# Performance work log

Measured on AMD Instinct MI355X. Metric: run time of the kernel, lower is better.

The kernel has to match this reference:

```python
import jax, jax.numpy as jnp
import numpy as np

H, D, K, FF = 8, 512, 64, 64  # n_head, feature_dim, key_feature_dim, dim_feedforward
L, B = 512, 32
LN_EPS = 1e-5


def _l2norm(x, eps=1e-12):
    # torch F.normalize: x / max(||x||, eps)
    n = jnp.sqrt(jnp.sum(x * x, axis=-1, keepdims=True))
    return x / jnp.maximum(n, eps)


def _layernorm(x, g, b, eps=LN_EPS):
    m = jnp.mean(x, axis=-1, keepdims=True)
    v = jnp.mean((x - m) ** 2, axis=-1, keepdims=True)
    return (x - m) * jax.lax.rsqrt(v + eps) * g + b


def setup_inputs() -> dict:
    key0 = jax.random.key(0)
    ks = jax.random.split(key0, 13)
    n = jax.random.normal
    s_kq = float(np.sqrt(2.0 / K))
    s_v = float(np.sqrt(2.0 / D))
    return {
        "query": n(ks[0], (L, B, D), jnp.float32),
        "key": n(ks[1], (L, B, D), jnp.float32),
        "value": n(ks[2], (L, B, D), jnp.float32),
        "WK": n(ks[3], (H, K, D), jnp.float32) * s_kq,
        "WQ": n(ks[4], (H, K, D), jnp.float32) * s_kq,
        "WV": n(ks[5], (H, D, D), jnp.float32) * s_v,
        "Wt": n(ks[6], (H, D, D), jnp.float32) * 0.04,  # trans_conv (default kaiming-ish scale)
        "W1": n(ks[7], (H, FF, D), jnp.float32) * 0.04,
        "b1": jnp.zeros((H, FF), jnp.float32),
        "W2": n(ks[8], (H, D, FF), jnp.float32) * 0.1,
        "b2": jnp.zeros((H, D), jnp.float32),
        "ln_g": jnp.ones((H, D), jnp.float32),
        "ln_b": jnp.zeros((H, D), jnp.float32),
    }


def reference(query, key, value, WK, WQ, WV, Wt, W1, b1, W2, b2, ln_g, ln_b):
    # query/key/value: [L, B, D]; per-head weights stacked on leading H axis.
    Lq, Bb, Dd = query.shape
    Hh = WK.shape[0]

    # per-head cosine-normalized Q/K projections: [H, B, L, K]
    wq = _l2norm(jnp.einsum('lbd,hkd->hblk', query, WQ))
    wk = _l2norm(jnp.einsum('lbd,hkd->hblk', key, WK))

    # attention scores [H, B, Lq, Lk], temp = 1
    dot = jnp.einsum('hbqc,hbkc->hbqk', wq, wk)
    aff = jax.nn.softmax(dot, axis=-1)
    # custom renorm: divide by column sums over the QUERY axis
    aff = aff / (1e-9 + jnp.sum(aff, axis=2, keepdims=True))

    wv = jnp.einsum('lbd,hed->hble', value, WV)        # [H, B, Lk, D]
    out = jnp.einsum('hbqk,hbke->hbqe', aff, wv)       # [H, B, Lq, D]
    out = jnp.transpose(out, (0, 2, 1, 3))             # [H, L, B, D]

    # residual-style trans_conv(query - out) -> relu
    o = jax.nn.relu(jnp.einsum('hlbd,hed->hlbe', query[None] - out, Wt))

    # TransNonlinear FFN (dropout = identity at eval)
    hff = jax.nn.relu(jnp.einsum('hlbd,hfd->hlbf', o, W1) + b1[:, None, None, :])
    s2 = jnp.einsum('hlbf,hdf->hlbd', hff, W2) + b2[:, None, None, :]
    x = _layernorm(o + s2, ln_g[:, None, None, :], ln_b[:, None, None, :])

    # concat heads on last dim, head 0 first: [L, B, H*D]
    return jnp.transpose(x, (1, 2, 0, 3)).reshape(Lq, Bb, Hh * Dd)
```

## Files before the change

### kernel.cpp

```cpp
#include <hip/hip_runtime.h>
#include <stdint.h>

#define HH 8
#define DDIM 512
#define KHEAD 64
#define FFD 64
#define LLEN 512
#define BBATCH 32
#define NTOK 16384

typedef unsigned short u16;
typedef __attribute__((ext_vector_type(8))) __bf16 bf16x8;
typedef __attribute__((ext_vector_type(4))) float f32x4;

__device__ __forceinline__ float bf2f(u16 u) {
    union { uint32_t i; float f; } v; v.i = ((uint32_t)u) << 16; return v.f;
}
__device__ __forceinline__ u16 f2bf(float f) {
    union { uint32_t i; float f; } v; v.f = f;
    return (u16)((v.i + 0x7FFFu + ((v.i >> 16) & 1u)) >> 16);
}

__device__ __forceinline__ void gload16(const void* g, void* l) {
    __builtin_amdgcn_global_load_lds(
        (const __attribute__((address_space(1))) void*)g,
        (__attribute__((address_space(3))) void*)l, 16, 0, 0);
}

struct ConvJob { const float* s; u16* d; int n4; };
struct ConvJobs { ConvJob j[6]; int nj; };

__global__ __launch_bounds__(256) void conv_multi(ConvJobs jobs) {
    for (int k = 0; k < jobs.nj; ++k) {
        const float* s = jobs.j[k].s;
        u16* d = jobs.j[k].d;
        const int n4 = jobs.j[k].n4;
        for (long i = (long)blockIdx.x * 256 + threadIdx.x; i < n4;
             i += (long)gridDim.x * 256) {
            float4 v = ((const float4*)s)[i];
            ushort4 o;
            o.x = f2bf(v.x); o.y = f2bf(v.y); o.z = f2bf(v.z); o.w = f2bf(v.w);
            ((ushort4*)d)[i] = o;
        }
    }
}

enum { M_PLAIN = 0, M_WQK = 1, M_SUBAUX = 2, M_RELU = 3, M_ADDAUX = 4, M_SCALECOL = 5 };

template<int MODE, int ZMAP, int SWAPXY>
__global__ __launch_bounds__(512) void mgemm256(
    const u16* __restrict__ A, const u16* __restrict__ B, u16* __restrict__ C,
    int Kd, int lda, int ldb, int ldc,
    long Ash, long Asb, long Bsh, long Bsb, long Csh, long Csb, int nB2,
    const float* __restrict__ bias, int biasN,
    const void* __restrict__ auxp, long auxsh, long auxsb, int auxld)
{
    __shared__ u16 As[2][256 * 64];
    __shared__ u16 Bs[2][256 * 64];

    const int z = blockIdx.z;
    int h2, b2;
    if (ZMAP == 0)      { h2 = z / nB2;      b2 = z % nB2; }
    else if (ZMAP == 1) { h2 = z & 7;        b2 = z >> 3; }
    else                { h2 = (z >> 3) & 7; b2 = ((z >> 6) << 3) | (z & 7); }
    const int bx = SWAPXY ? blockIdx.y : blockIdx.x;
    const int by = SWAPXY ? blockIdx.x : blockIdx.y;
    const int m0 = bx * 256, n0 = by * 256;
    const u16* Ab = A + h2 * Ash + b2 * Asb + (long)m0 * lda;
    const u16* Bb = B + h2 * Bsh + b2 * Bsb + (long)n0 * ldb;

    const int t = threadIdx.x;
    const int lane = t & 63;
    const int w = t >> 6;
    const int wm = w >> 2;
    const int wn = w & 3;
    const int l15 = lane & 15;
    const int g = lane >> 4;

    f32x4 acc[8][4];
    #pragma unroll
    for (int mf = 0; mf < 8; ++mf)
        #pragma unroll
        for (int nf = 0; nf < 4; ++nf)
            #pragma unroll
            for (int i = 0; i < 4; ++i) acc[mf][nf][i] = 0.f;

    auto stageT = [&](int buf, int k0) {
        #pragma unroll
        for (int c = 0; c < 4; ++c) {
            const int idx = c * 8192 + t * 16;
            const int row = idx >> 7;
            const int g0 = (idx >> 4) & 7;
            gload16((const char*)(Ab + (long)row * lda + k0) + ((g0 ^ (row & 7)) << 4),
                    (char*)As[buf] + c * 8192 + w * 1024);
        }
        #pragma unroll
        for (int c = 0; c < 4; ++c) {
            const int idx = c * 8192 + t * 16;
            const int row = idx >> 7;
            const int g0 = (idx >> 4) & 7;
            gload16((const char*)(Bb + (long)row * ldb + k0) + ((g0 ^ (row & 7)) << 4),
                    (char*)Bs[buf] + c * 8192 + w * 1024);
        }
    };

    stageT(0, 0);
    const int nt = Kd >> 6;
    for (int T = 0; T < nt; ++T) {
        asm volatile("s_waitcnt vmcnt(0)" ::: "memory");
        __builtin_amdgcn_sched_barrier(0);
        __builtin_amdgcn_s_barrier();
        __builtin_amdgcn_sched_barrier(0);
        if (T + 1 < nt) stageT((T + 1) & 1, (T + 1) << 6);

        const char* Abase = (const char*)As[T & 1];
        const char* Bbase = (const char*)Bs[T & 1];
        #pragma unroll
        for (int q = 0; q < 4; ++q) {
            const int mh = q >> 1, nh = q & 1;
            bf16x8 af[4][2], bfv[2][2];
            #pragma unroll
            for (int mf = 0; mf < 4; ++mf) {
                const int row = wm * 128 + (mh * 4 + mf) * 16 + l15;
                #pragma unroll
                for (int kk = 0; kk < 2; ++kk)
                    af[mf][kk] = *(const bf16x8*)(Abase + row * 128 +
                                      (((kk * 4 + g) ^ (row & 7)) << 4));
            }
            #pragma unroll
            for (int nf = 0; nf < 2; ++nf) {
                const int row = wn * 64 + (nh * 2 + nf) * 16 + l15;
                #pragma unroll
                for (int kk = 0; kk < 2; ++kk)
                    bfv[nf][kk] = *(const bf16x8*)(Bbase + row * 128 +
                                      (((kk * 4 + g) ^ (row & 7)) << 4));
            }
            __builtin_amdgcn_s_setprio(1);
            #pragma unroll
            for (int kk = 0; kk < 2; ++kk)
                #pragma unroll
                for (int mf = 0; mf < 4; ++mf)
                    #pragma unroll
                    for (int nf = 0; nf < 2; ++nf)
                        acc[mh * 4 + mf][nh * 2 + nf] =
                            __builtin_amdgcn_mfma_f32_16x16x32_bf16(
                                af[mf][kk], bfv[nf][kk],
                                acc[mh * 4 + mf][nh * 2 + nf], 0, 0, 0);
            __builtin_amdgcn_s_setprio(0);
            __builtin_amdgcn_sched_barrier(0);
        }
    }

    const int lr = g * 4;
    const int lc = l15;
    const long cof = h2 * Csh + b2 * Csb;
    #pragma unroll
    for (int mf = 0; mf < 8; ++mf) {
        #pragma unroll
        for (int i = 0; i < 4; ++i) {
            const int r = m0 + wm * 128 + mf * 16 + lr + i;
            #pragma unroll
            for (int nf = 0; nf < 4; ++nf) {
                const int c = n0 + wn * 64 + nf * 16 + lc;
                float v = acc[mf][nf][i];
                if (MODE == M_SUBAUX) {
                    const u16* q = (const u16*)auxp;
                    v = bf2f(q[auxsh * h2 + auxsb * b2 + (long)r * auxld + c]) - v;
                } else if (MODE == M_RELU) {
                    if (bias) v += bias[h2 * biasN + c];
                    v = fmaxf(v, 0.0f);
                } else if (MODE == M_SCALECOL) {
                    const float* cs = (const float*)auxp + auxsh * h2 + auxsb * b2;
                    v *= 1.0f / (1e-9f + cs[c]);
                }
                C[cof + (long)r * ldc + c] = f2bf(v);
            }
        }
    }
}

template<int BM, int BN, int MODE, int ZMAP, int SWAPXY>
__global__ __launch_bounds__(256) void mgemm(
    const u16* __restrict__ A, const u16* __restrict__ B, u16* __restrict__ C,
    int Kd, int lda, int ldb, int ldc,
    long Ash, long Asb, long Bsh, long Bsb, long Csh, long Csb, int nB2,
    const float* __restrict__ bias, int biasN,
    const void* __restrict__ auxp, long auxsh, long auxsb, int auxld)
{
    constexpr int WC = (BN == 128) ? 2 : 1;
    constexpr int WR = 4 / WC;
    constexpr int WTM = BM / WR;
    constexpr int WTN = BN / WC;
    constexpr int MF = WTM / 16;
    constexpr int NF = WTN / 16;
    constexpr int NCA = (BM * 64) / 4096;
    constexpr int NCB = (BN * 64) / 4096;
    __shared__ u16 As[2][BM * 32];
    __shared__ u16 Bs[2][BN * 32];

    const int z = blockIdx.z;
    int h2, b2;
    if (ZMAP == 0)      { h2 = z / nB2;      b2 = z % nB2; }
    else if (ZMAP == 1) { h2 = z & 7;        b2 = z >> 3; }
    else                { h2 = (z >> 3) & 7; b2 = ((z >> 6) << 3) | (z & 7); }
    const u16* Ab = A + h2 * Ash + b2 * Asb;
    const u16* Bb = B + h2 * Bsh + b2 * Bsb;
    const int bx = SWAPXY ? blockIdx.y : blockIdx.x;
    const int by = SWAPXY ? blockIdx.x : blockIdx.y;
    const int m0 = bx * BM, n0 = by * BN;
    const int t = threadIdx.x;
    const int lane = t & 63;
    const int w = t >> 6;
    const int wr = w / WC, wc = w % WC;
    const int tb = t * 16;
    const int wb = (t & 192) * 16;

    f32x4 acc[MF][NF];
    #pragma unroll
    for (int m = 0; m < MF; ++m)
        #pragma unroll
        for (int n = 0; n < NF; ++n)
            #pragma unroll
            for (int i = 0; i < 4; ++i) acc[m][n][i] = 0.f;

    const int ko = (lane >> 4) * 16;

    auto stage = [&](int buf, int k0) {
        #pragma unroll
        for (int c = 0; c < NCA; ++c) {
            const int byte = c * 4096 + tb;
            const int row = byte >> 6;
            gload16((const char*)(Ab + (long)(m0 + row) * lda + k0) + (byte & 63),
                    (char*)As[buf] + c * 4096 + wb);
        }
        #pragma unroll
        for (int c = 0; c < NCB; ++c) {
            const int byte = c * 4096 + tb;
            const int row = byte >> 6;
            gload16((const char*)(Bb + (long)(n0 + row) * ldb + k0) + (byte & 63),
                    (char*)Bs[buf] + c * 4096 + wb);
        }
    };

    stage(0, 0);
    __syncthreads();
    int cur = 0;
    const int nsteps = Kd >> 5;
    for (int s = 0; s < nsteps; ++s) {
        if (s + 1 < nsteps) stage(cur ^ 1, (s + 1) << 5);
        bf16x8 af[MF], bfr[NF];
        #pragma unroll
        for (int m = 0; m < MF; ++m)
            af[m] = *(const bf16x8*)((const char*)As[cur] + (wr * WTM + m * 16 + (lane & 15)) * 64 + ko);
        #pragma unroll
        for (int n = 0; n < NF; ++n)
            bfr[n] = *(const bf16x8*)((const char*)Bs[cur] + (wc * WTN + n * 16 + (lane & 15)) * 64 + ko);
        #pragma unroll
        for (int m = 0; m < MF; ++m)
            #pragma unroll
            for (int n = 0; n < NF; ++n)
                acc[m][n] = __builtin_amdgcn_mfma_f32_16x16x32_bf16(af[m], bfr[n], acc[m][n], 0, 0, 0);
        __syncthreads();
        cur ^= 1;
    }

    const int lr = (lane >> 4) * 4;
    const int lc = lane & 15;

    if constexpr (MODE == M_WQK) {
        const int h = (n0 + wc * WTN) >> 6;
        #pragma unroll
        for (int m = 0; m < MF; ++m) {
            #pragma unroll
            for (int i = 0; i < 4; ++i) {
                float s = 0.f;
                #pragma unroll
                for (int n = 0; n < NF; ++n) { const float v = acc[m][n][i]; s += v * v; }
                s += __shfl_xor(s, 1); s += __shfl_xor(s, 2);
                s += __shfl_xor(s, 4); s += __shfl_xor(s, 8);
                const float inv = 1.0f / fmaxf(sqrtf(s), 1e-12f);
                const int r = m0 + wr * WTM + m * 16 + lr + i;
                const int l = r >> 5, bq = r & 31;
                const int sw = (l & 7) << 3;
                u16* rowp = C + (((long)(h * BBATCH + bq) * LLEN + l) * KHEAD);
                #pragma unroll
                for (int n = 0; n < NF; ++n)
                    rowp[(lc + n * 16) ^ sw] = f2bf(acc[m][n][i] * inv);
            }
        }
    } else {
        const long cof = h2 * Csh + b2 * Csb;
        #pragma unroll
        for (int m = 0; m < MF; ++m) {
            #pragma unroll
            for (int i = 0; i < 4; ++i) {
                const int r = m0 + wr * WTM + m * 16 + lr + i;
                #pragma unroll
                for (int n = 0; n < NF; ++n) {
                    const int c = n0 + wc * WTN + n * 16 + lc;
                    float v = acc[m][n][i];
                    if (MODE == M_SUBAUX) {
                        const u16* q = (const u16*)auxp;
                        v = bf2f(q[auxsh * h2 + auxsb * b2 + (long)r * auxld + c]) - v;
                    } else if (MODE == M_RELU) {
                        if (bias) v += bias[h2 * biasN + c];
                        v = fmaxf(v, 0.0f);
                    } else if (MODE == M_ADDAUX) {
                        v += bias[h2 * biasN + c];
                        const u16* ax = (const u16*)auxp;
                        v += bf2f(ax[auxsh * h2 + auxsb * b2 + (long)r * auxld + c]);
                    } else if (MODE == M_SCALECOL) {
                        const float* cs = (const float*)auxp + auxsh * h2 + auxsb * b2;
                        v *= 1.0f / (1e-9f + cs[c]);
                    }
                    C[cof + (long)r * ldc + c] = f2bf(v);
                }
            }
        }
    }
}

__device__ __forceinline__ void xcd_decode(int wgid, int& qt, int& b, int& h) {
    const int r = wgid & 7;
    const int inner = wgid >> 3;
    qt = inner & 7;
    h = (inner >> 3) & 7;
    b = ((inner >> 6) << 3) | r;
}

__global__ __launch_bounds__(256) void attn_mfma(
    const u16* __restrict__ wq, const u16* __restrict__ wk,
    u16* __restrict__ P, float* __restrict__ colsum)
{
    __shared__ u16 qs[64 * 64];
    __shared__ u16 ks[512 * 64];
    __shared__ float smax[4][64];
    __shared__ float ssum[4][64];

    int qt, b, h;
    xcd_decode(blockIdx.x, qt, b, h);
    const long hb = h * BBATCH + b;
    const int t = threadIdx.x;
    const int lane = t & 63, w = t >> 6;
    const int wb = (t & 192) * 16;

    const char* qg = (const char*)(wq + (hb * LLEN + qt * 64) * KHEAD);
    const char* kg = (const char*)(wk + hb * LLEN * KHEAD);
    #pragma unroll
    for (int c = 0; c < 2; ++c)
        gload16(qg + c * 4096 + t * 16, (char*)qs + c * 4096 + wb);
    #pragma unroll
    for (int c = 0; c < 16; ++c)
        gload16(kg + c * 4096 + t * 16, (char*)ks + c * 4096 + wb);
    __syncthreads();

    const int l15 = lane & 15;
    const int g = lane >> 4;
    const int swz = (lane & 7) << 4;

    f32x4 acc[4][8];
    #pragma unroll
    for (int m = 0; m < 4; ++m)
        #pragma unroll
        for (int n = 0; n < 8; ++n)
            #pragma unroll
            for (int i = 0; i < 4; ++i) acc[m][n][i] = 0.f;

    #pragma unroll
    for (int kk = 0; kk < 2; ++kk) {
        bf16x8 af[4];
        #pragma unroll
        for (int m = 0; m < 4; ++m) {
            const int row = m * 16 + l15;
            af[m] = *(const bf16x8*)((const char*)qs + row * 128 + ((g * 16 + kk * 64) ^ swz));
        }
        #pragma unroll
        for (int n = 0; n < 8; ++n) {
            const int row = (w * 8 + n) * 16 + l15;
            const bf16x8 bfr = *(const bf16x8*)((const char*)ks + row * 128 + ((g * 16 + kk * 64) ^ swz));
            #pragma unroll
            for (int m = 0; m < 4; ++m)
                acc[m][n] = __builtin_amdgcn_mfma_f32_16x16x32_bf16(af[m], bfr, acc[m][n], 0, 0, 0);
        }
    }

    float rmax[4][4];
    #pragma unroll
    for (int m = 0; m < 4; ++m)
        #pragma unroll
        for (int i = 0; i < 4; ++i) {
            float mx = acc[m][0][i];
            #pragma unroll
            for (int n = 1; n < 8; ++n) mx = fmaxf(mx, acc[m][n][i]);
            mx = fmaxf(mx, __shfl_xor(mx, 1));
            mx = fmaxf(mx, __shfl_xor(mx, 2));
            mx = fmaxf(mx, __shfl_xor(mx, 4));
            mx = fmaxf(mx, __shfl_xor(mx, 8));
            if (l15 == 0) smax[w][m * 16 + g * 4 + i] = mx;
        }
    __syncthreads();
    #pragma unroll
    for (int m = 0; m < 4; ++m)
        #pragma unroll
        for (int i = 0; i < 4; ++i) {
            const int r = m * 16 + g * 4 + i;
            rmax[m][i] = fmaxf(fmaxf(smax[0][r], smax[1][r]),
                               fmaxf(smax[2][r], smax[3][r]));
        }
    float rinv[4][4];
    #pragma unroll
    for (int m = 0; m < 4; ++m)
        #pragma unroll
        for (int i = 0; i < 4; ++i) {
            float s = 0.f;
            #pragma unroll
            for (int n = 0; n < 8; ++n) {
                acc[m][n][i] = __expf(acc[m][n][i] - rmax[m][i]);
                s += acc[m][n][i];
            }
            s += __shfl_xor(s, 1); s += __shfl_xor(s, 2);
            s += __shfl_xor(s, 4); s += __shfl_xor(s, 8);
            if (l15 == 0) ssum[w][m * 16 + g * 4 + i] = s;
        }
    __syncthreads();
    #pragma unroll
    for (int m = 0; m < 4; ++m)
        #pragma unroll
        for (int i = 0; i < 4; ++i) {
            const int r = m * 16 + g * 4 + i;
            rinv[m][i] = 1.0f / (ssum[0][r] + ssum[1][r] + ssum[2][r] + ssum[3][r]);
        }

    u16* Pb = P + (hb * LLEN + qt * 64) * LLEN + w * 128;
    float cs[8];
    #pragma unroll
    for (int n = 0; n < 8; ++n) cs[n] = 0.f;
    #pragma unroll
    for (int m = 0; m < 4; ++m)
        #pragma unroll
        for (int i = 0; i < 4; ++i) {
            const int r = m * 16 + g * 4 + i;
            u16* pr = Pb + (long)r * LLEN + l15;
            const float iv = rinv[m][i];
            #pragma unroll
            for (int n = 0; n < 8; ++n) {
                const float p = acc[m][n][i] * iv;
                pr[n * 16] = f2bf(p);
                cs[n] += p;
            }
        }
    #pragma unroll
    for (int n = 0; n < 8; ++n) {
        cs[n] += __shfl_xor(cs[n], 16);
        cs[n] += __shfl_xor(cs[n], 32);
    }
    if (lane < 16) {
        float* cb = colsum + hb * 512 + w * 128 + lane;
        #pragma unroll
        for (int n = 0; n < 8; ++n) atomicAdd(&cb[n * 16], cs[n]);
    }
}

__global__ __launch_bounds__(256) void ffn2_ln(
    const u16* __restrict__ hff, const u16* __restrict__ W2bf,
    const float* __restrict__ b2, const u16* __restrict__ o,
    const float* __restrict__ lng, const float* __restrict__ lnb,
    float* __restrict__ out)
{
    __shared__ u16 W2s[512 * 64];
    __shared__ u16 hs[32 * 64];
    __shared__ float redS[4][32];
    __shared__ float redQ[4][32];

    const int h = blockIdx.z;
    const int m0 = blockIdx.x * 32;
    const int t = threadIdx.x;
    const int lane = t & 63, w = t >> 6;
    const int l15 = lane & 15, g = lane >> 4;
    const int wb = (t & 192) * 16;

    const char* w2g = (const char*)W2bf + (long)h * 65536;
    #pragma unroll
    for (int c = 0; c < 16; ++c) {
        const int idx = c * 4096 + t * 16;
        const int row = idx >> 7;
        const int g0 = (idx >> 4) & 7;
        gload16(w2g + row * 128 + ((g0 ^ (row & 7)) << 4),
                (char*)W2s + c * 4096 + wb);
    }
    {
        const int idx = t * 16;
        const int row = idx >> 7;
        const int g0 = (idx >> 4) & 7;
        gload16((const char*)(hff + ((long)h * NTOK + m0) * FFD) +
                    row * 128 + ((g0 ^ (row & 7)) << 4),
                (char*)hs + wb);
    }
    __syncthreads();

    f32x4 acc[2][8];
    #pragma unroll
    for (int m = 0; m < 2; ++m)
        #pragma unroll
        for (int n = 0; n < 8; ++n)
            #pragma unroll
            for (int i = 0; i < 4; ++i) acc[m][n][i] = 0.f;

    #pragma unroll
    for (int kk = 0; kk < 2; ++kk) {
        bf16x8 af[2];
        #pragma unroll
        for (int m = 0; m < 2; ++m) {
            const int row = m * 16 + l15;
            af[m] = *(const bf16x8*)((const char*)hs + row * 128 +
                                     (((kk * 4 + g) ^ (row & 7)) << 4));
        }
        #pragma unroll
        for (int n = 0; n < 8; ++n) {
            const int e = w * 128 + n * 16 + l15;
            const bf16x8 bfr = *(const bf16x8*)((const char*)W2s + e * 128 +
                                                (((kk * 4 + g) ^ (e & 7)) << 4));
            #pragma unroll
            for (int m = 0; m < 2; ++m)
                acc[m][n] = __builtin_amdgcn_mfma_f32_16x16x32_bf16(af[m], bfr, acc[m][n], 0, 0, 0);
        }
    }

    float b2v[8], gv[8], bv[8];
    #pragma unroll
    for (int n = 0; n < 8; ++n) {
        const int c = w * 128 + n * 16 + l15;
        b2v[n] = b2[h * DDIM + c];
        gv[n] = lng[h * DDIM + c];
        bv[n] = lnb[h * DDIM + c];
    }
    const u16* ob = o + ((long)h * NTOK + m0) * DDIM;
    #pragma unroll
    for (int m = 0; m < 2; ++m)
        #pragma unroll
        for (int i = 0; i < 4; ++i) {
            const int row = m * 16 + g * 4 + i;
            float s = 0.f, q = 0.f;
            #pragma unroll
            for (int n = 0; n < 8; ++n) {
                const int c = w * 128 + n * 16 + l15;
                const float v = acc[m][n][i] + b2v[n] + bf2f(ob[(long)row * DDIM + c]);
                acc[m][n][i] = v;
                s += v; q += v * v;
            }
            s += __shfl_xor(s, 1); q += __shfl_xor(q, 1);
            s += __shfl_xor(s, 2); q += __shfl_xor(q, 2);
            s += __shfl_xor(s, 4); q += __shfl_xor(q, 4);
            s += __shfl_xor(s, 8); q += __shfl_xor(q, 8);
            if (l15 == 0) { redS[w][row] = s; redQ[w][row] = q; }
        }
    __syncthreads();

    #pragma unroll
    for (int m = 0; m < 2; ++m)
        #pragma unroll
        for (int i = 0; i < 4; ++i) {
            const int row = m * 16 + g * 4 + i;
            const float s = redS[0][row] + redS[1][row] + redS[2][row] + redS[3][row];
            const float q = redQ[0][row] + redQ[1][row] + redQ[2][row] + redQ[3][row];
            const float mu = s * (1.0f / 512.0f);
            const float var = q * (1.0f / 512.0f) - mu * mu;
            const float rs = rsqrtf(var + 1e-5f);
            const int tok = m0 + row;
            const int b = tok >> 9, l = tok & 511;
            float* op = out + ((long)(l * BBATCH + b)) * (HH * DDIM) + h * DDIM;
            #pragma unroll
            for (int n = 0; n < 8; ++n) {
                const int c = w * 128 + n * 16 + l15;
                op[c] = (acc[m][n][i] - mu) * rs * gv[n] + bv[n];
            }
        }
}

extern "C" void kernel_launch(void* const* d_in, const int* in_sizes, int n_in,
                              void* d_out, int out_size, void* d_ws, size_t ws_size,
                              hipStream_t stream) {
    const float* query = (const float*)d_in[0];
    const float* key   = (const float*)d_in[1];
    const float* value = (const float*)d_in[2];
    const float* WK = (const float*)d_in[3];
    const float* WQ = (const float*)d_in[4];
    const float* WV = (const float*)d_in[5];
    const float* Wt = (const float*)d_in[6];
    const float* W1 = (const float*)d_in[7];
    const float* b1 = (const float*)d_in[8];
    const float* W2 = (const float*)d_in[9];
    const float* b2 = (const float*)d_in[10];
    const float* lng = (const float*)d_in[11];
    const float* lnb = (const float*)d_in[12];

    char* ws = (char*)d_ws;
    u16* kbf  = (u16*)(ws);
    u16* WQbf = (u16*)(ws + 16777216);
    u16* WKbf = (u16*)(ws + 17301504);
    u16* P    = (u16*)(ws);
    u16* vbf  = (u16*)(ws + 134217728);
    u16* WVbf = (u16*)(ws + 150994944);
    u16* o    = (u16*)(ws + 134217728);
    float* colsum = (float*)(ws + 268435456);
    u16* qbf  = (u16*)(ws + 268959744);
    u16* hff  = qbf;
    u16* wq   = (u16*)(ws + 285736960);
    u16* wk   = (u16*)(ws + 302514176);
    u16* Wtbf = (u16*)(ws + 285736960);
    u16* W1bf = (u16*)(ws + 289931264);
    u16* W2bf = (u16*)(ws + 290455552);
    u16* qmo = (u16*)d_out;
    u16* wvT = (u16*)((char*)d_out + 134217728);

    if (ws_size < 319291392u) return;

    hipMemsetAsync(colsum, 0, 524288, stream);
    const dim3 blk(256);

    {
        ConvJobs J;
        J.j[0] = { query, qbf, 2097152 };
        J.j[1] = { key,   kbf, 2097152 };
        J.j[2] = { value, vbf, 2097152 };
        J.j[3] = { WQ, WQbf, 65536 };
        J.j[4] = { WK, WKbf, 65536 };
        J.j[5] = { WV, WVbf, 524288 };
        J.nj = 6;
        conv_multi<<<dim3(2048), blk, 0, stream>>>(J);
    }

    mgemm<128, 128, M_WQK, 0, 1><<<dim3(4, 128, 1), blk, 0, stream>>>(
        qbf, WQbf, wq, 512, 512, 512, 0,
        0, 0, 0, 0, 0, 0, 1, nullptr, 0, nullptr, 0, 0, 0);
    mgemm<128, 128, M_WQK, 0, 1><<<dim3(4, 128, 1), blk, 0, stream>>>(
        kbf, WKbf, wk, 512, 512, 512, 0,
        0, 0, 0, 0, 0, 0, 1, nullptr, 0, nullptr, 0, 0, 0);

    attn_mfma<<<dim3(2048), blk, 0, stream>>>(wq, wk, P, colsum);

    {
        ConvJobs J;
        J.j[0] = { Wt, Wtbf, 524288 };
        J.j[1] = { W1, W1bf, 65536 };
        J.j[2] = { W2, W2bf, 65536 };
        J.nj = 3;
        conv_multi<<<dim3(1024), blk, 0, stream>>>(J);
    }

    mgemm256<M_SCALECOL, 2, 0><<<dim3(2, 2, 256), dim3(512), 0, stream>>>(
        WVbf, vbf, wvT, 512, 512, BBATCH * DDIM, 512,
        (long)DDIM * DDIM, 0, 0, DDIM,
        (long)BBATCH * DDIM * LLEN, (long)DDIM * LLEN, 32,
        nullptr, 0, colsum, (long)BBATCH * 512, 512, 0);

    mgemm256<M_SUBAUX, 1, 0><<<dim3(2, 2, 256), dim3(512), 0, stream>>>(
        P, wvT, qmo, 512, 512, 512, 512,
        (long)BBATCH * LLEN * LLEN, (long)LLEN * LLEN,
        (long)BBATCH * DDIM * LLEN, (long)DDIM * LLEN,
        (long)BBATCH * LLEN * DDIM, (long)LLEN * DDIM, 32,
        nullptr, 0, qbf, 0, DDIM, BBATCH * DDIM);

    mgemm256<M_RELU, 0, 1><<<dim3(2, 64, 8), dim3(512), 0, stream>>>(
        qmo, Wtbf, o, 512, 512, 512, 512,
        (long)NTOK * DDIM, 0, (long)DDIM * DDIM, 0,
        (long)NTOK * DDIM, 0, 1, nullptr, 512, nullptr, 0, 0, 0);

    mgemm<128, 64, M_RELU, 0, 0><<<dim3(128, 1, 8), blk, 0, stream>>>(
        o, W1bf, hff, 512, 512, 512, 64,
        (long)NTOK * DDIM, 0, (long)FFD * DDIM, 0,
        (long)NTOK * FFD, 0, 1, b1, 64, nullptr, 0, 0, 0);

    ffn2_ln<<<dim3(512, 1, 8), blk, 0, stream>>>(hff, W2bf, b2, o, lng, lnb,
                                                 (float*)d_out);
}
```

Baseline: 746.4 us.

## Split 256x256 GEMM tiles into half-tiles with fine-grained staged prefetch

Restructures the 256x256 MFMA GEMM so the A and B shared tiles are split into 128-row halves, each loaded separately and consumed in four phases per K step. Prefetches for the next K step are interleaved between the phases using partial vmcnt waits instead of a full drain, so global-to-LDS loads overlap with MFMA work. Each wave's output tile is remapped to a 2x2 set of 64x32 sub-tiles across the halves. This adds more barriers per K step and relies on hand-counted vmcnt values being correct.

After: 762.9 us. 2.2% more time.

```diff
diff --git a/kernel.cpp b/kernel.cpp
--- a/kernel.cpp
+++ b/kernel.cpp
@@ -47,16 +47,42 @@
 
 enum { M_PLAIN = 0, M_WQK = 1, M_SUBAUX = 2, M_RELU = 3, M_ADDAUX = 4, M_SCALECOL = 5 };
 
+#define PHASE(ah, bh)  do {                                                    \
+    const char* Abase = (const char*)As[pb][ah];                               \
+    const char* Bbase = (const char*)Bs[pb][bh];                               \
+    bf16x8 af[4][2], bfv[2][2];                                                \
+    _Pragma("unroll") for (int mf = 0; mf < 4; ++mf) {                         \
+        const int rl = wr * 64 + mf * 16 + l15;                                \
+        _Pragma("unroll") for (int kk = 0; kk < 2; ++kk)                       \
+            af[mf][kk] = *(const bf16x8*)(Abase + rl * 128 +                   \
+                               (((kk * 4 + g) ^ (rl & 7)) << 4));              \
+    }                                                                          \
+    _Pragma("unroll") for (int nf = 0; nf < 2; ++nf) {                         \
+        const int rl = wc * 32 + nf * 16 + l15;                                \
+        _Pragma("unroll") for (int kk = 0; kk < 2; ++kk)                       \
+            bfv[nf][kk] = *(const bf16x8*)(Bbase + rl * 128 +                  \
+                               (((kk * 4 + g) ^ (rl & 7)) << 4));              \
+    }                                                                          \
+    __builtin_amdgcn_s_setprio(1);                                             \
+    _Pragma("unroll") for (int kk = 0; kk < 2; ++kk)                           \
+        _Pragma("unroll") for (int mf = 0; mf < 4; ++mf)                       \
+            _Pragma("unroll") for (int nf = 0; nf < 2; ++nf)                   \
+                acc[ah][bh][mf][nf] = __builtin_amdgcn_mfma_f32_16x16x32_bf16( \
+                    af[mf][kk], bfv[nf][kk], acc[ah][bh][mf][nf], 0, 0, 0);    \
+    __builtin_amdgcn_s_setprio(0);                                             \
+    __builtin_amdgcn_sched_barrier(0);                                         \
+} while (0)
+
 template<int MODE, int ZMAP, int SWAPXY>
-__global__ __launch_bounds__(512) void mgemm256(
+__global__ __launch_bounds__(512) void mgemm256p(
     const u16* __restrict__ A, const u16* __restrict__ B, u16* __restrict__ C,
     int Kd, int lda, int ldb, int ldc,
     long Ash, long Asb, long Bsh, long Bsb, long Csh, long Csb, int nB2,
     const float* __restrict__ bias, int biasN,
     const void* __restrict__ auxp, long auxsh, long auxsb, int auxld)
 {
-    __shared__ u16 As[2][256 * 64];
-    __shared__ u16 Bs[2][256 * 64];
+    __shared__ u16 As[2][2][128 * 64];
+    __shared__ u16 Bs[2][2][128 * 64];
 
     const int z = blockIdx.z;
     int h2, b2;
@@ -72,111 +98,114 @@
     const int t = threadIdx.x;
     const int lane = t & 63;
     const int w = t >> 6;
-    const int wm = w >> 2;
-    const int wn = w & 3;
+    const int wr = w >> 2;
+    const int wc = w & 3;
     const int l15 = lane & 15;
     const int g = lane >> 4;
 
-    f32x4 acc[8][4];
-    #pragma unroll
-    for (int mf = 0; mf < 8; ++mf)
-        #pragma unroll
-        for (int nf = 0; nf < 4; ++nf)
-            #pragma unroll
-            for (int i = 0; i < 4; ++i) acc[mf][nf][i] = 0.f;
-
-    auto stageT = [&](int buf, int k0) {
-        #pragma unroll
-        for (int c = 0; c < 4; ++c) {
+    f32x4 acc[2][2][4][2];
+    #pragma unroll
+    for (int a = 0; a < 2; ++a)
+        #pragma unroll
+        for (int b = 0; b < 2; ++b)
+            #pragma unroll
+            for (int m = 0; m < 4; ++m)
+                #pragma unroll
+                for (int n = 0; n < 2; ++n)
+                    #pragma unroll
+                    for (int i = 0; i < 4; ++i) acc[a][b][m][n][i] = 0.f;
+
+    auto SA = [&](int buf, int half, int k0) {
+        #pragma unroll
+        for (int c = 0; c < 2; ++c) {
             const int idx = c * 8192 + t * 16;
             const int row = idx >> 7;
             const int g0 = (idx >> 4) & 7;
-            gload16((const char*)(Ab + (long)row * lda + k0) + ((g0 ^ (row & 7)) << 4),
-                    (char*)As[buf] + c * 8192 + w * 1024);
-        }
-        #pragma unroll
-        for (int c = 0; c < 4; ++c) {
+            gload16((const char*)(Ab + (long)(half * 128 + row) * lda + k0) +
+                        ((g0 ^ (row & 7)) << 4),
+                    (char*)As[buf][half] + c * 8192 + w * 1024);
+        }
+    };
+    auto SB = [&](int buf, int half, int k0) {
+        #pragma unroll
+        for (int c = 0; c < 2; ++c) {
             const int idx = c * 8192 + t * 16;
             const int row = idx >> 7;
             const int g0 = (idx >> 4) & 7;
-            gload16((const char*)(Bb + (long)row * ldb + k0) + ((g0 ^ (row & 7)) << 4),
-                    (char*)Bs[buf] + c * 8192 + w * 1024);
+            gload16((const char*)(Bb + (long)(half * 128 + row) * ldb + k0) +
+                        ((g0 ^ (row & 7)) << 4),
+                    (char*)Bs[buf][half] + c * 8192 + w * 1024);
         }
     };
 
-    stageT(0, 0);
     const int nt = Kd >> 6;
+    SA(0, 0, 0); SB(0, 0, 0); SA(0, 1, 0); SB(0, 1, 0);
+    if (nt > 1) SA(1, 0, 64);
+
     for (int T = 0; T < nt; ++T) {
-        asm volatile("s_waitcnt vmcnt(0)" ::: "memory");
+        const int pb = T & 1;
+        const int k1 = (T + 1) << 6;
+        const bool pf = (T + 1) < nt;
+
+        if (pf) SB(pb ^ 1, 0, k1);
+        if (pf) asm volatile("s_waitcnt vmcnt(8)" ::: "memory");
+        else    asm volatile("s_waitcnt vmcnt(4)" ::: "memory");
         __builtin_amdgcn_sched_barrier(0);
         __builtin_amdgcn_s_barrier();
         __builtin_amdgcn_sched_barrier(0);
-        if (T + 1 < nt) stageT((T + 1) & 1, (T + 1) << 6);
-
-        const char* Abase = (const char*)As[T & 1];
-        const char* Bbase = (const char*)Bs[T & 1];
-        #pragma unroll
-        for (int q = 0; q < 4; ++q) {
-            const int mh = q >> 1, nh = q & 1;
-            bf16x8 af[4][2], bfv[2][2];
-            #pragma unroll
-            for (int mf = 0; mf < 4; ++mf) {
-                const int row = wm * 128 + (mh * 4 + mf) * 16 + l15;
+        PHASE(0, 0);
+
+        if (pf) SA(pb ^ 1, 1, k1);
+        if (pf) asm volatile("s_waitcnt vmcnt(8)" ::: "memory");
+        else    asm volatile("s_waitcnt vmcnt(2)" ::: "memory");
+        __builtin_amdgcn_sched_barrier(0);
+        __builtin_amdgcn_s_barrier();
+        __builtin_amdgcn_sched_barrier(0);
+        PHASE(1, 0);
+
+        if (pf) SB(pb ^ 1, 1, k1);
+        if (pf) asm volatile("s_waitcnt vmcnt(8)" ::: "memory");
+        else    asm volatile("s_waitcnt vmcnt(0)" ::: "memory");
+        __builtin_amdgcn_sched_barrier(0);
+        __builtin_amdgcn_s_barrier();
+        __builtin_amdgcn_sched_barrier(0);
+        PHASE(0, 1);
+
+        __builtin_amdgcn_sched_barrier(0);
+        __builtin_amdgcn_s_barrier();
+        __builtin_amdgcn_sched_barrier(0);
+        if (T + 2 < nt) SA(pb, 0, (T + 2) << 6);
+        PHASE(1, 1);
+    }
+
+    const int lr = g * 4;
+    const long cof = h2 * Csh + b2 * Csb;
+    #pragma unroll
+    for (int ah = 0; ah < 2; ++ah)
+        #pragma unroll
+        for (int bh = 0; bh < 2; ++bh)
+            #pragma unroll
+            for (int mf = 0; mf < 4; ++mf)
                 #pragma unroll
-                for (int kk = 0; kk < 2; ++kk)
-                    af[mf][kk] = *(const bf16x8*)(Abase + row * 128 +
-                                      (((kk * 4 + g) ^ (row & 7)) << 4));
-            }
-            #pragma unroll
-            for (int nf = 0; nf < 2; ++nf) {
-                const int row = wn * 64 + (nh * 2 + nf) * 16 + l15;
-                #pragma unroll
-                for (int kk = 0; kk < 2; ++kk)
-                    bfv[nf][kk] = *(const bf16x8*)(Bbase + row * 128 +
-                                      (((kk * 4 + g) ^ (row & 7)) << 4));
-            }
-            __builtin_amdgcn_s_setprio(1);
-            #pragma unroll
-            for (int kk = 0; kk < 2; ++kk)
-                #pragma unroll
-                for (int mf = 0; mf < 4; ++mf)
+                for (int i = 0; i < 4; ++i) {
+                    const int r = m0 + ah * 128 + wr * 64 + mf * 16 + lr + i;
                     #pragma unroll
-                    for (int nf = 0; nf < 2; ++nf)
-                        acc[mh * 4 + mf][nh * 2 + nf] =
-                            __builtin_amdgcn_mfma_f32_16x16x32_bf16(
-                                af[mf][kk], bfv[nf][kk],
-                                acc[mh * 4 + mf][nh * 2 + nf], 0, 0, 0);
-            __builtin_amdgcn_s_setprio(0);
-            __builtin_amdgcn_sched_barrier(0);
-        }
-    }
-
-    const int lr = g * 4;
-    const int lc = l15;
-    const long cof = h2 * Csh + b2 * Csb;
-    #pragma unroll
-    for (int mf = 0; mf < 8; ++mf) {
-        #pragma unroll
-        for (int i = 0; i < 4; ++i) {
-            const int r = m0 + wm * 128 + mf * 16 + lr + i;
-            #pragma unroll
-            for (int nf = 0; nf < 4; ++nf) {
-                const int c = n0 + wn * 64 + nf * 16 + lc;
-                float v = acc[mf][nf][i];
-                if (MODE == M_SUBAUX) {
-                    const u16* q = (const u16*)auxp;
-                    v = bf2f(q[auxsh * h2 + auxsb * b2 + (long)r * auxld + c]) - v;
-                } else if (MODE == M_RELU) {
-                    if (bias) v += bias[h2 * biasN + c];
-                    v = fmaxf(v, 0.0f);
-                } else if (MODE == M_SCALECOL) {
-                    const float* cs = (const float*)auxp + auxsh * h2 + auxsb * b2;
-                    v *= 1.0f / (1e-9f + cs[c]);
+                    for (int nf = 0; nf < 2; ++nf) {
+                        const int c = n0 + bh * 128 + wc * 32 + nf * 16 + l15;
+                        float v = acc[ah][bh][mf][nf][i];
+                        if (MODE == M_SUBAUX) {
+                            const u16* q = (const u16*)auxp;
+                            v = bf2f(q[auxsh * h2 + auxsb * b2 + (long)r * auxld + c]) - v;
+                        } else if (MODE == M_RELU) {
+                            if (bias) v += bias[h2 * biasN + c];
+                            v = fmaxf(v, 0.0f);
+                        } else if (MODE == M_SCALECOL) {
+                            const float* cs = (const float*)auxp + auxsh * h2 + auxsb * b2;
+                            v *= 1.0f / (1e-9f + cs[c]);
+                        }
+                        C[cof + (long)r * ldc + c] = f2bf(v);
+                    }
                 }
-                C[cof + (long)r * ldc + c] = f2bf(v);
-            }
-        }
-    }
 }
 
 template<int BM, int BN, int MODE, int ZMAP, int SWAPXY>
@@ -648,20 +677,20 @@
         conv_multi<<<dim3(1024), blk, 0, stream>>>(J);
     }
 
-    mgemm256<M_SCALECOL, 2, 0><<<dim3(2, 2, 256), dim3(512), 0, stream>>>(
+    mgemm256p<M_SCALECOL, 2, 0><<<dim3(2, 2, 256), dim3(512), 0, stream>>>(
         WVbf, vbf, wvT, 512, 512, BBATCH * DDIM, 512,
         (long)DDIM * DDIM, 0, 0, DDIM,
         (long)BBATCH * DDIM * LLEN, (long)DDIM * LLEN, 32,
         nullptr, 0, colsum, (long)BBATCH * 512, 512, 0);
 
-    mgemm256<M_SUBAUX, 1, 0><<<dim3(2, 2, 256), dim3(512), 0, stream>>>(
+    mgemm256p<M_SUBAUX, 1, 0><<<dim3(2, 2, 256), dim3(512), 0, stream>>>(
         P, wvT, qmo, 512, 512, 512, 512,
         (long)BBATCH * LLEN * LLEN, (long)LLEN * LLEN,
         (long)BBATCH * DDIM * LLEN, (long)DDIM * LLEN,
         (long)BBATCH * LLEN * DDIM, (long)LLEN * DDIM, 32,
         nullptr, 0, qbf, 0, DDIM, BBATCH * DDIM);
 
-    mgemm256<M_RELU, 0, 1><<<dim3(2, 64, 8), dim3(512), 0, stream>>>(
+    mgemm256p<M_RELU, 0, 1><<<dim3(2, 64, 8), dim3(512), 0, stream>>>(
         qmo, Wtbf, o, 512, 512, 512, 512,
         (long)NTOK * DDIM, 0, (long)DDIM * DDIM, 0,
         (long)NTOK * DDIM, 0, 1, nullptr, 512, nullptr, 0, 0, 0);
```

## Halve K-tile of 256x256 GEMM to 32 and restructure double-buffer sync

Applied to the files above, without the earlier changes.

The 256x256 bf16 GEMM now stages K in 32-wide tiles instead of 64, which halves LDS use per buffer (64KB to 32KB total) and changes the XOR swizzle to a 4-group pattern. The main loop issues the next tile's global-to-LDS loads before computing the current tile and uses __syncthreads at the end of each iteration, replacing the explicit vmcnt wait plus barrier at the top. It also drops the four-quadrant sub-blocking and does all 32 MFMAs per step in one pass. The lower LDS footprint may allow higher occupancy, but the cost is twice as many barriers and iterations. The in-loop synchronization may not cover the async global_load_lds completion properly.

Measured after the change: 780.8 us. +4.6%, slower.

```diff
diff --git a/kernel.cpp b/kernel.cpp
--- a/kernel.cpp
+++ b/kernel.cpp
@@ -48,15 +48,15 @@
 enum { M_PLAIN = 0, M_WQK = 1, M_SUBAUX = 2, M_RELU = 3, M_ADDAUX = 4, M_SCALECOL = 5 };
 
 template<int MODE, int ZMAP, int SWAPXY>
-__global__ __launch_bounds__(512) void mgemm256(
+__global__ __launch_bounds__(512) void mgemm256s(
     const u16* __restrict__ A, const u16* __restrict__ B, u16* __restrict__ C,
     int Kd, int lda, int ldb, int ldc,
     long Ash, long Asb, long Bsh, long Bsb, long Csh, long Csb, int nB2,
     const float* __restrict__ bias, int biasN,
     const void* __restrict__ auxp, long auxsh, long auxsb, int auxld)
 {
-    __shared__ u16 As[2][256 * 64];
-    __shared__ u16 Bs[2][256 * 64];
+    __shared__ u16 As[2][256 * 32];
+    __shared__ u16 Bs[2][256 * 32];
 
     const int z = blockIdx.z;
     int h2, b2;
@@ -87,72 +87,55 @@
 
     auto stageT = [&](int buf, int k0) {
         #pragma unroll
-        for (int c = 0; c < 4; ++c) {
+        for (int c = 0; c < 2; ++c) {
             const int idx = c * 8192 + t * 16;
-            const int row = idx >> 7;
-            const int g0 = (idx >> 4) & 7;
-            gload16((const char*)(Ab + (long)row * lda + k0) + ((g0 ^ (row & 7)) << 4),
+            const int row = idx >> 6;
+            const int g0 = (idx >> 4) & 3;
+            gload16((const char*)(Ab + (long)row * lda + k0) + ((g0 ^ (row & 3)) << 4),
                     (char*)As[buf] + c * 8192 + w * 1024);
         }
         #pragma unroll
-        for (int c = 0; c < 4; ++c) {
+        for (int c = 0; c < 2; ++c) {
             const int idx = c * 8192 + t * 16;
-            const int row = idx >> 7;
-            const int g0 = (idx >> 4) & 7;
-            gload16((const char*)(Bb + (long)row * ldb + k0) + ((g0 ^ (row & 7)) << 4),
+            const int row = idx >> 6;
+            const int g0 = (idx >> 4) & 3;
+            gload16((const char*)(Bb + (long)row * ldb + k0) + ((g0 ^ (row & 3)) << 4),
                     (char*)Bs[buf] + c * 8192 + w * 1024);
         }
     };
 
     stageT(0, 0);
-    const int nt = Kd >> 6;
+    __syncthreads();
+    const int nt = Kd >> 5;
+    int cur = 0;
     for (int T = 0; T < nt; ++T) {
-        asm volatile("s_waitcnt vmcnt(0)" ::: "memory");
-        __builtin_amdgcn_sched_barrier(0);
-        __builtin_amdgcn_s_barrier();
-        __builtin_amdgcn_sched_barrier(0);
-        if (T + 1 < nt) stageT((T + 1) & 1, (T + 1) << 6);
-
-        const char* Abase = (const char*)As[T & 1];
-        const char* Bbase = (const char*)Bs[T & 1];
-        #pragma unroll
-        for (int q = 0; q < 4; ++q) {
-            const int mh = q >> 1, nh = q & 1;
-            bf16x8 af[4][2], bfv[2][2];
-            #pragma unroll
-            for (int mf = 0; mf < 4; ++mf) {
-                const int row = wm * 128 + (mh * 4 + mf) * 16 + l15;
-                #pragma unroll
-                for (int kk = 0; kk < 2; ++kk)
-                    af[mf][kk] = *(const bf16x8*)(Abase + row * 128 +
-                                      (((kk * 4 + g) ^ (row & 7)) << 4));
-            }
-            #pragma unroll
-            for (int nf = 0; nf < 2; ++nf) {
-                const int row = wn * 64 + (nh * 2 + nf) * 16 + l15;
-                #pragma unroll
-                for (int kk = 0; kk < 2; ++kk)
-                    bfv[nf][kk] = *(const bf16x8*)(Bbase + row * 128 +
-                                      (((kk * 4 + g) ^ (row & 7)) << 4));
-            }
-            __builtin_amdgcn_s_setprio(1);
-            #pragma unroll
-            for (int kk = 0; kk < 2; ++kk)
-                #pragma unroll
-                for (int mf = 0; mf < 4; ++mf)
-                    #pragma unroll
-                    for (int nf = 0; nf < 2; ++nf)
-                        acc[mh * 4 + mf][nh * 2 + nf] =
-                            __builtin_amdgcn_mfma_f32_16x16x32_bf16(
-                                af[mf][kk], bfv[nf][kk],
-                                acc[mh * 4 + mf][nh * 2 + nf], 0, 0, 0);
-            __builtin_amdgcn_s_setprio(0);
-            __builtin_amdgcn_sched_barrier(0);
-        }
+        if (T + 1 < nt) stageT(cur ^ 1, (T + 1) << 5);
+        const char* Abase = (const char*)As[cur];
+        const char* Bbase = (const char*)Bs[cur];
+        bf16x8 af[8], bfv[4];
+        #pragma unroll
+        for (int mf = 0; mf < 8; ++mf) {
+            const int row = wm * 128 + mf * 16 + l15;
+            af[mf] = *(const bf16x8*)(Abase + row * 64 + ((g ^ (row & 3)) << 4));
+        }
+        #pragma unroll
+        for (int nf = 0; nf < 4; ++nf) {
+            const int row = wn * 64 + nf * 16 + l15;
+            bfv[nf] = *(const bf16x8*)(Bbase + row * 64 + ((g ^ (row & 3)) << 4));
+        }
+        __builtin_amdgcn_s_setprio(1);
+        #pragma unroll
+        for (int mf = 0; mf < 8; ++mf)
+            #pragma unroll
+            for (int nf = 0; nf < 4; ++nf)
+                acc[mf][nf] = __builtin_amdgcn_mfma_f32_16x16x32_bf16(
+                    af[mf], bfv[nf], acc[mf][nf], 0, 0, 0);
+        __builtin_amdgcn_s_setprio(0);
+        __syncthreads();
+        cur ^= 1;
     }
 
     const int lr = g * 4;
-    const int lc = l15;
     const long cof = h2 * Csh + b2 * Csb;
     #pragma unroll
     for (int mf = 0; mf < 8; ++mf) {
@@ -161,7 +144,7 @@
             const int r = m0 + wm * 128 + mf * 16 + lr + i;
             #pragma unroll
             for (int nf = 0; nf < 4; ++nf) {
-                const int c = n0 + wn * 64 + nf * 16 + lc;
+                const int c = n0 + wn * 64 + nf * 16 + l15;
                 float v = acc[mf][nf][i];
                 if (MODE == M_SUBAUX) {
                     const u16* q = (const u16*)auxp;
@@ -648,20 +631,20 @@
         conv_multi<<<dim3(1024), blk, 0, stream>>>(J);
     }
 
-    mgemm256<M_SCALECOL, 2, 0><<<dim3(2, 2, 256), dim3(512), 0, stream>>>(
+    mgemm256s<M_SCALECOL, 2, 0><<<dim3(2, 2, 256), dim3(512), 0, stream>>>(
         WVbf, vbf, wvT, 512, 512, BBATCH * DDIM, 512,
         (long)DDIM * DDIM, 0, 0, DDIM,
         (long)BBATCH * DDIM * LLEN, (long)DDIM * LLEN, 32,
         nullptr, 0, colsum, (long)BBATCH * 512, 512, 0);
 
-    mgemm256<M_SUBAUX, 1, 0><<<dim3(2, 2, 256), dim3(512), 0, stream>>>(
+    mgemm256s<M_SUBAUX, 1, 0><<<dim3(2, 2, 256), dim3(512), 0, stream>>>(
         P, wvT, qmo, 512, 512, 512, 512,
         (long)BBATCH * LLEN * LLEN, (long)LLEN * LLEN,
         (long)BBATCH * DDIM * LLEN, (long)DDIM * LLEN,
         (long)BBATCH * LLEN * DDIM, (long)LLEN * DDIM, 32,
         nullptr, 0, qbf, 0, DDIM, BBATCH * DDIM);
 
-    mgemm256<M_RELU, 0, 1><<<dim3(2, 64, 8), dim3(512), 0, stream>>>(
+    mgemm256s<M_RELU, 0, 1><<<dim3(2, 64, 8), dim3(512), 0, stream>>>(
         qmo, Wtbf, o, 512, 512, 512, 512,
         (long)NTOK * DDIM, 0, (long)DDIM * DDIM, 0,
         (long)NTOK * DDIM, 0, 1, nullptr, 512, nullptr, 0, 0, 0);
```
